# Kernel optimization log

Measured on AMD Instinct MI355X. Metric: run time of the kernel, lower is better.

## Reference

```python
import jax, jax.numpy as jnp
import numpy as np

N_STAGES = 400
N_CLASSES = 10          # trees per stage (dimension)
DEPTH = 6               # complete binary trees: 63 internal nodes, 64 leaves
N_TREES = N_STAGES * N_CLASSES
N_INTERNAL = 2 ** DEPTH - 1
N_LEAVES = 2 ** DEPTH
N_FEATURES = 128
BATCH = 32768
LEARNING_RATE = 0.1


def setup_inputs() -> dict:
    key = jax.random.key(0)
    k1, k2, k3, k4, k5 = jax.random.split(key, 5)
    x = jax.random.normal(k1, (BATCH, N_FEATURES), dtype=jnp.float32)
    features = jax.random.randint(k2, (N_TREES, N_INTERNAL), 0, N_FEATURES, dtype=jnp.int32)
    thresholds = jax.random.normal(k3, (N_TREES, N_INTERNAL), dtype=jnp.float32)
    leaf_values = jax.random.normal(k4, (N_TREES, N_LEAVES), dtype=jnp.float32) * 0.1
    init_out = jax.random.normal(k5, (N_CLASSES,), dtype=jnp.float32)
    return {"x": x, "features": features, "thresholds": thresholds,
            "leaf_values": leaf_values, "init_out": init_out}


def reference(x, features, thresholds, leaf_values, init_out):
    # Batched evaluation of all trees of all boosting stages at once
    # (fused form of: out = init + lr * sum_stages stack([tree(x) for tree in stage])).
    N = x.shape[0]
    T = features.shape[0]
    t_idx = jnp.arange(T)[None, :]                       # [1, T]
    idx = jnp.zeros((N, T), dtype=jnp.int32)             # current node per (sample, tree)
    for _ in range(DEPTH):
        f = features[t_idx, idx]                         # [N, T] feature id at node
        thr = thresholds[t_idx, idx]                     # [N, T]
        xv = jnp.take_along_axis(x, f, axis=1)           # [N, T] feature value
        # left child if x <= thr, right child otherwise (sklearn convention)
        idx = 2 * idx + 1 + (xv > thr).astype(jnp.int32)
    leaf = idx - N_INTERNAL                              # [N, T] leaf index
    vals = leaf_values[t_idx, leaf]                      # [N, T] raw tree outputs
    per_stage = vals.reshape(N, N_STAGES, N_CLASSES)     # [N, S, K]
    out = init_out[None, :] + LEARNING_RATE * per_stage.sum(axis=1)  # [N, K]
    return out
```

## Files before the change

### kernel.cpp

```cpp
#include <hip/hip_runtime.h>
#include <stdint.h>

#define N_CLASSES  10
#define N_TREES    4000
#define DEPTH      6
#define N_INTERNAL 63
#define N_FEATURES 128
#define BATCH      32768
#define LR         0.1f

#define BLOCK       256
#define SAMPLES_PB  32
#define T_TILE      16
#define N_TILES     (N_TREES / T_TILE)
#define TILES_PER_CLASS ((N_TREES / N_CLASSES) / T_TILE)
#define SUMS_STRIDE 11

#define WS_NODES_BYTES  ((size_t)N_TREES * 64 * 8)
#define WS_LEAVES_BYTES ((size_t)N_TREES * 64 * 4)

#define WAITCNT_VM4  0x0F74
#define WAITCNT_VM2  0x0F72

__global__ void pack_kernel(const int* __restrict__ features,
                            const float* __restrict__ thresholds,
                            const float* __restrict__ leaves,
                            int2* __restrict__ pn, float* __restrict__ pl) {
    int i = blockIdx.x * blockDim.x + threadIdx.x;
    int t = i >> 6, n = i & 63;
    if (t < N_TREES) {
        int slot = (t % N_CLASSES) * (N_TREES / N_CLASSES) + (t / N_CLASSES);
        if (n < N_INTERNAL)
            pn[slot * 64 + n] = make_int2(features[t * N_INTERNAL + n],
                                          __float_as_int(thresholds[t * N_INTERNAL + n]));
        pl[slot * 64 + n] = leaves[t * 64 + n];
    }
}

__device__ __forceinline__ void load_lds_16(const void* g, void* l) {
    const auto* g1 = reinterpret_cast<const __attribute__((address_space(1))) uint32_t*>(
        reinterpret_cast<uintptr_t>(g));
    auto* l3 = reinterpret_cast<__attribute__((address_space(3))) uint32_t*>(
        reinterpret_cast<uintptr_t>(l));
    __builtin_amdgcn_global_load_lds(g1, l3, 16, 0, 0);
}

template <bool XT>
__global__ __launch_bounds__(BLOCK, 4) void gbt_eval(
    const float* __restrict__ x,
    const float* __restrict__ xt,
    const int2*  __restrict__ pnodes,
    const float* __restrict__ pleaves,
    const float* __restrict__ init_out,
    float*       __restrict__ out)
{
    __shared__ float xs[N_FEATURES * SAMPLES_PB];
    __shared__ int2  nbuf[2][T_TILE * 64];
    __shared__ float sums[SAMPLES_PB * SUMS_STRIDE];

    const int tid = threadIdx.x;
    const int sample0 = blockIdx.x * SAMPLES_PB;
    const int lane    = tid & 63;
    const int wv      = tid >> 6;

    if (XT) {
        #pragma unroll
        for (int q = 0; q < 4; ++q) {
            int f0 = wv * 32 + q * 8;
            const char* g = (const char*)(xt
                + (size_t)(f0 + (lane >> 3)) * BATCH + sample0 + (lane & 7) * 4);
            load_lds_16(g, (char*)xs + (size_t)f0 * SAMPLES_PB * 4);
        }
    } else {
        const float4* xg = (const float4*)(x + (size_t)sample0 * N_FEATURES);
        for (int e = tid; e < SAMPLES_PB * (N_FEATURES / 4); e += BLOCK) {
            int s = e >> 5, f4 = e & 31;
            float4 v = xg[e];
            int f = f4 << 2;
            xs[(f + 0) * SAMPLES_PB + s] = v.x;
            xs[(f + 1) * SAMPLES_PB + s] = v.y;
            xs[(f + 2) * SAMPLES_PB + s] = v.z;
            xs[(f + 3) * SAMPLES_PB + s] = v.w;
        }
    }
    for (int i = tid; i < SAMPLES_PB * SUMS_STRIDE; i += BLOCK) sums[i] = 0.f;

    auto stage = [&](int tile, int b) {
        const char* g = (const char*)(pnodes + (size_t)(tile * T_TILE) * 64);
        char* lbase = (char*)&nbuf[b][0];
        #pragma unroll
        for (int q = 0; q < 2; ++q) {
            int k = wv * 2 + q;
            load_lds_16(g + k * 1024 + lane * 16, lbase + k * 1024);
        }
    };

    stage(0, 0);
    __syncthreads();

    const int sLocal = tid & (SAMPLES_PB - 1);
    const int j      = tid >> 5;

    int cur = 0;
    for (int c = 0; c < N_CLASSES; ++c) {
        float acc = 0.f;
        float lv0 = 0.f, lv1 = 0.f;
        for (int t25 = 0; t25 < TILES_PER_CLASS; ++t25) {
            const int tile = c * TILES_PER_CLASS + t25;
            if (tile + 1 < N_TILES) {
                stage(tile + 1, cur ^ 1);
                __builtin_amdgcn_s_waitcnt(WAITCNT_VM4);
            } else {
                __builtin_amdgcn_s_waitcnt(WAITCNT_VM2);
            }

            const int2* nb0 = &nbuf[cur][(j * 2 + 0) * 64];
            const int2* nb1 = &nbuf[cur][(j * 2 + 1) * 64];
            int o0 = 0, o1 = 0;
            #pragma unroll
            for (int d = 0; d < DEPTH; ++d) {
                int2 a = nb0[o0];
                int2 b = nb1[o1];
                float x0 = xs[a.x * SAMPLES_PB + sLocal];
                float x1 = xs[b.x * SAMPLES_PB + sLocal];
                o0 = 2 * o0 + 1 + (x0 > __int_as_float(a.y) ? 1 : 0);
                o1 = 2 * o1 + 1 + (x1 > __int_as_float(b.y) ? 1 : 0);
            }
            const size_t slotA = (size_t)(tile * T_TILE + j * 2);
            acc += lv0 + lv1;
            lv0 = pleaves[slotA * 64       + (o0 - N_INTERNAL)];
            lv1 = pleaves[(slotA + 1) * 64 + (o1 - N_INTERNAL)];
            cur ^= 1;
        }
        acc += lv0 + lv1;
        atomicAdd(&sums[sLocal * SUMS_STRIDE + c], acc);
    }
    __syncthreads();

    for (int e = tid; e < SAMPLES_PB * N_CLASSES; e += BLOCK) {
        int s = e / N_CLASSES, k = e - s * N_CLASSES;
        out[(size_t)(sample0 + s) * N_CLASSES + k] =
            init_out[k] + LR * sums[s * SUMS_STRIDE + k];
    }
}

__global__ __launch_bounds__(BLOCK, 8) void gbt_eval_global(
    const float* __restrict__ x,
    const int*   __restrict__ features,
    const float* __restrict__ thresholds,
    const float* __restrict__ leaf_values,
    const float* __restrict__ init_out,
    float*       __restrict__ out)
{
    __shared__ float xs[N_FEATURES * SAMPLES_PB];
    __shared__ float sums[SAMPLES_PB * N_CLASSES];
    const int tid = threadIdx.x;
    const int sample0 = blockIdx.x * SAMPLES_PB;
    {
        const float4* xg = (const float4*)(x + (size_t)sample0 * N_FEATURES);
        for (int e = tid; e < SAMPLES_PB * (N_FEATURES / 4); e += BLOCK) {
            int s = e >> 5, f4 = e & 31;
            float4 v = xg[e];
            int f = f4 << 2;
            xs[(f + 0) * SAMPLES_PB + s] = v.x;
            xs[(f + 1) * SAMPLES_PB + s] = v.y;
            xs[(f + 2) * SAMPLES_PB + s] = v.z;
            xs[(f + 3) * SAMPLES_PB + s] = v.w;
        }
    }
    for (int i = tid; i < SAMPLES_PB * N_CLASSES; i += BLOCK) sums[i] = 0.f;
    __syncthreads();
    const int sLocal = tid & (SAMPLES_PB - 1);
    const int j = tid >> 5;
    const int TPT = N_TREES / 8;
    const int t0 = j * TPT;
    float acc[N_CLASSES];
    #pragma unroll
    for (int k = 0; k < N_CLASSES; ++k) acc[k] = 0.f;
    for (int i = 0; i < TPT; i += N_CLASSES) {
        const int tt = t0 + i;
        int idx[N_CLASSES];
        #pragma unroll
        for (int u = 0; u < N_CLASSES; ++u) idx[u] = 0;
        #pragma unroll
        for (int d = 0; d < DEPTH; ++d) {
            #pragma unroll
            for (int u = 0; u < N_CLASSES; ++u) {
                int base = (tt + u) * N_INTERNAL + idx[u];
                float xv = xs[features[base] * SAMPLES_PB + sLocal];
                idx[u] = 2 * idx[u] + 1 + (xv > thresholds[base] ? 1 : 0);
            }
        }
        #pragma unroll
        for (int u = 0; u < N_CLASSES; ++u)
            acc[u] += leaf_values[(size_t)(tt + u) * 64 + idx[u] - N_INTERNAL];
    }
    #pragma unroll
    for (int k = 0; k < N_CLASSES; ++k)
        atomicAdd(&sums[sLocal * N_CLASSES + k], acc[k]);
    __syncthreads();
    for (int e = tid; e < SAMPLES_PB * N_CLASSES; e += BLOCK) {
        int s = e / N_CLASSES, k = e - s * N_CLASSES;
        out[(size_t)(sample0 + s) * N_CLASSES + k] = init_out[k] + LR * sums[e];
    }
}

extern "C" void kernel_launch(void* const* d_in, const int* in_sizes, int n_in,
                              void* d_out, int out_size, void* d_ws, size_t ws_size,
                              hipStream_t stream) {
    const float* x          = (const float*)d_in[0];
    const int*   features   = (const int*)d_in[1];
    const float* thresholds = (const float*)d_in[2];
    const float* leafvals   = (const float*)d_in[3];
    const float* init_out   = (const float*)d_in[4];
    float*       out        = (float*)d_out;

    const int grid = BATCH / SAMPLES_PB;

    if (ws_size >= WS_NODES_BYTES + WS_LEAVES_BYTES) {
        int2*  pn = (int2*)d_ws;
        float* pl = (float*)((char*)d_ws + WS_NODES_BYTES);
        int n = N_TREES * 64;
        pack_kernel<<<(n + 255) / 256, 256, 0, stream>>>(features, thresholds,
                                                         leafvals, pn, pl);
        gbt_eval<false><<<grid, BLOCK, 0, stream>>>(x, nullptr, pn, pl, init_out, out);
    } else {
        gbt_eval_global<<<BATCH / SAMPLES_PB, BLOCK, 0, stream>>>(
            x, features, thresholds, leafvals, init_out, out);
    }
}
```

Baseline: 293.2 us.

## Fuse node packing into eval kernel via cooperative grid sync

Moves the tree node and leaf packing step into the main evaluation kernel. Each block packs its share of nodes, then all blocks wait at a cooperative grid-wide barrier before running tree traversal. This removes a separate kernel launch and the gap between the two launches. In exchange it needs every block resident at once (1024 blocks at 4 per CU) and pays for a grid barrier. If the cooperative launch fails, it falls back to the old two-kernel path.

```diff
diff --git a/kernel.cpp b/kernel.cpp
--- a/kernel.cpp
+++ b/kernel.cpp
@@ -1,5 +1,8 @@
 #include <hip/hip_runtime.h>
+#include <hip/hip_cooperative_groups.h>
 #include <stdint.h>
+
+namespace cg = cooperative_groups;
 
 #define N_CLASSES  10
 #define N_TREES    4000
@@ -21,6 +24,122 @@
 
 #define WAITCNT_VM4  0x0F74
 #define WAITCNT_VM2  0x0F72
+
+__device__ __forceinline__ void load_lds_16(const void* g, void* l) {
+    const auto* g1 = reinterpret_cast<const __attribute__((address_space(1))) uint32_t*>(
+        reinterpret_cast<uintptr_t>(g));
+    auto* l3 = reinterpret_cast<__attribute__((address_space(3))) uint32_t*>(
+        reinterpret_cast<uintptr_t>(l));
+    __builtin_amdgcn_global_load_lds(g1, l3, 16, 0, 0);
+}
+
+__global__ __launch_bounds__(BLOCK, 4) void gbt_fused(
+    const float* __restrict__ x,
+    const int*   __restrict__ features,
+    const float* __restrict__ thresholds,
+    const float* __restrict__ leaves,
+    const float* __restrict__ init_out,
+    float*       __restrict__ out,
+    int2*        __restrict__ pnodes,
+    float*       __restrict__ pleaves)
+{
+    __shared__ float xs[N_FEATURES * SAMPLES_PB];
+    __shared__ int2  nbuf[2][T_TILE * 64];
+    __shared__ float sums[SAMPLES_PB * SUMS_STRIDE];
+
+    const int tid = threadIdx.x;
+    const int sample0 = blockIdx.x * SAMPLES_PB;
+    const int lane    = tid & 63;
+    const int wv      = tid >> 6;
+
+    {
+        const float4* xg = (const float4*)(x + (size_t)sample0 * N_FEATURES);
+        for (int e = tid; e < SAMPLES_PB * (N_FEATURES / 4); e += BLOCK) {
+            int s = e >> 5, f4 = e & 31;
+            float4 v = xg[e];
+            int f = f4 << 2;
+            xs[(f + 0) * SAMPLES_PB + s] = v.x;
+            xs[(f + 1) * SAMPLES_PB + s] = v.y;
+            xs[(f + 2) * SAMPLES_PB + s] = v.z;
+            xs[(f + 3) * SAMPLES_PB + s] = v.w;
+        }
+    }
+    for (int i = tid; i < SAMPLES_PB * SUMS_STRIDE; i += BLOCK) sums[i] = 0.f;
+
+    {
+        int i = blockIdx.x * BLOCK + tid;
+        int t = i >> 6, n = i & 63;
+        if (t < N_TREES) {
+            int slot = (t % N_CLASSES) * (N_TREES / N_CLASSES) + (t / N_CLASSES);
+            if (n < N_INTERNAL)
+                pnodes[slot * 64 + n] =
+                    make_int2(features[t * N_INTERNAL + n],
+                              __float_as_int(thresholds[t * N_INTERNAL + n]));
+            pleaves[slot * 64 + n] = leaves[t * 64 + n];
+        }
+    }
+
+    __threadfence();
+    cg::this_grid().sync();
+
+    auto stage = [&](int tile, int b) {
+        const char* g = (const char*)(pnodes + (size_t)(tile * T_TILE) * 64);
+        char* lbase = (char*)&nbuf[b][0];
+        #pragma unroll
+        for (int q = 0; q < 2; ++q) {
+            int k = wv * 2 + q;
+            load_lds_16(g + k * 1024 + lane * 16, lbase + k * 1024);
+        }
+    };
+
+    stage(0, 0);
+    __syncthreads();
+
+    const int sLocal = tid & (SAMPLES_PB - 1);
+    const int j      = tid >> 5;
+
+    int cur = 0;
+    for (int c = 0; c < N_CLASSES; ++c) {
+        float acc = 0.f;
+        float lv0 = 0.f, lv1 = 0.f;
+        for (int t25 = 0; t25 < TILES_PER_CLASS; ++t25) {
+            const int tile = c * TILES_PER_CLASS + t25;
+            if (tile + 1 < N_TILES) {
+                stage(tile + 1, cur ^ 1);
+                __builtin_amdgcn_s_waitcnt(WAITCNT_VM4);
+            } else {
+                __builtin_amdgcn_s_waitcnt(WAITCNT_VM2);
+            }
+
+            const int2* nb0 = &nbuf[cur][(j * 2 + 0) * 64];
+            const int2* nb1 = &nbuf[cur][(j * 2 + 1) * 64];
+            int o0 = 0, o1 = 0;
+            #pragma unroll
+            for (int d = 0; d < DEPTH; ++d) {
+                int2 a = nb0[o0];
+                int2 b = nb1[o1];
+                float x0 = xs[a.x * SAMPLES_PB + sLocal];
+                float x1 = xs[b.x * SAMPLES_PB + sLocal];
+                o0 = 2 * o0 + 1 + (x0 > __int_as_float(a.y) ? 1 : 0);
+                o1 = 2 * o1 + 1 + (x1 > __int_as_float(b.y) ? 1 : 0);
+            }
+            const size_t slotA = (size_t)(tile * T_TILE + j * 2);
+            acc += lv0 + lv1;
+            lv0 = pleaves[slotA * 64       + (o0 - N_INTERNAL)];
+            lv1 = pleaves[(slotA + 1) * 64 + (o1 - N_INTERNAL)];
+            cur ^= 1;
+        }
+        acc += lv0 + lv1;
+        atomicAdd(&sums[sLocal * SUMS_STRIDE + c], acc);
+    }
+    __syncthreads();
+
+    for (int e = tid; e < SAMPLES_PB * N_CLASSES; e += BLOCK) {
+        int s = e / N_CLASSES, k = e - s * N_CLASSES;
+        out[(size_t)(sample0 + s) * N_CLASSES + k] =
+            init_out[k] + LR * sums[s * SUMS_STRIDE + k];
+    }
+}
 
 __global__ void pack_kernel(const int* __restrict__ features,
                             const float* __restrict__ thresholds,
@@ -37,18 +156,8 @@
     }
 }
 
-__device__ __forceinline__ void load_lds_16(const void* g, void* l) {
-    const auto* g1 = reinterpret_cast<const __attribute__((address_space(1))) uint32_t*>(
-        reinterpret_cast<uintptr_t>(g));
-    auto* l3 = reinterpret_cast<__attribute__((address_space(3))) uint32_t*>(
-        reinterpret_cast<uintptr_t>(l));
-    __builtin_amdgcn_global_load_lds(g1, l3, 16, 0, 0);
-}
-
-template <bool XT>
 __global__ __launch_bounds__(BLOCK, 4) void gbt_eval(
     const float* __restrict__ x,
-    const float* __restrict__ xt,
     const int2*  __restrict__ pnodes,
     const float* __restrict__ pleaves,
     const float* __restrict__ init_out,
@@ -63,15 +172,7 @@
     const int lane    = tid & 63;
     const int wv      = tid >> 6;
 
-    if (XT) {
-        #pragma unroll
-        for (int q = 0; q < 4; ++q) {
-            int f0 = wv * 32 + q * 8;
-            const char* g = (const char*)(xt
-                + (size_t)(f0 + (lane >> 3)) * BATCH + sample0 + (lane & 7) * 4);
-            load_lds_16(g, (char*)xs + (size_t)f0 * SAMPLES_PB * 4);
-        }
-    } else {
+    {
         const float4* xg = (const float4*)(x + (size_t)sample0 * N_FEATURES);
         for (int e = tid; e < SAMPLES_PB * (N_FEATURES / 4); e += BLOCK) {
             int s = e >> 5, f4 = e & 31;
@@ -113,7 +214,6 @@
             } else {
                 __builtin_amdgcn_s_waitcnt(WAITCNT_VM2);
             }
-
             const int2* nb0 = &nbuf[cur][(j * 2 + 0) * 64];
             const int2* nb1 = &nbuf[cur][(j * 2 + 1) * 64];
             int o0 = 0, o1 = 0;
@@ -220,10 +320,18 @@
     if (ws_size >= WS_NODES_BYTES + WS_LEAVES_BYTES) {
         int2*  pn = (int2*)d_ws;
         float* pl = (float*)((char*)d_ws + WS_NODES_BYTES);
-        int n = N_TREES * 64;
-        pack_kernel<<<(n + 255) / 256, 256, 0, stream>>>(features, thresholds,
-                                                         leafvals, pn, pl);
-        gbt_eval<false><<<grid, BLOCK, 0, stream>>>(x, nullptr, pn, pl, init_out, out);
+
+        void* args[] = {(void*)&x, (void*)&features, (void*)&thresholds,
+                        (void*)&leafvals, (void*)&init_out, (void*)&out,
+                        (void*)&pn, (void*)&pl};
+        hipError_t err = hipLaunchCooperativeKernel(
+            (const void*)gbt_fused, dim3(grid), dim3(BLOCK), args, 0, stream);
+        if (err != hipSuccess) {
+            int n = N_TREES * 64;
+            pack_kernel<<<(n + 255) / 256, 256, 0, stream>>>(
+                features, thresholds, leafvals, pn, pl);
+            gbt_eval<<<grid, BLOCK, 0, stream>>>(x, pn, pl, init_out, out);
+        }
     } else {
         gbt_eval_global<<<BATCH / SAMPLES_PB, BLOCK, 0, stream>>>(
             x, features, thresholds, leafvals, init_out, out);
```

New measurement: 510.3 us. 74.0% more time.
